# Kernel optimization log

Measured on AMD Instinct MI355X. Metric: run time of the kernel, lower is better.

## Reference

```python
import jax, jax.numpy as jnp
import numpy as np

B, S, E, H, F = 4, 2048, 1024, 16, 4096
D = E // H
EPS = 1e-5


def setup_inputs() -> dict:
    key = jax.random.key(0)
    ks = jax.random.split(key, 12)
    sc_e = 1.0 / np.sqrt(E)
    sc_f = 1.0 / np.sqrt(F)
    inp = {
        'x': jax.random.normal(ks[0], (B, S, E), jnp.float32),
        'mask': jnp.tril(jnp.ones((S, S), jnp.int32))[None, None],  # causal [1,1,S,S]
        'ln1_g': jnp.ones((E,), jnp.float32),
        'ln1_b': jnp.zeros((E,), jnp.float32),
        'Wq': jax.random.normal(ks[1], (E, E), jnp.float32) * sc_e,
        'bq': jnp.zeros((E,), jnp.float32),
        'Wk': jax.random.normal(ks[2], (E, E), jnp.float32) * sc_e,
        'bk': jnp.zeros((E,), jnp.float32),
        'Wv': jax.random.normal(ks[3], (E, E), jnp.float32) * sc_e,
        'bv': jnp.zeros((E,), jnp.float32),
        'Wo': jax.random.normal(ks[4], (E, E), jnp.float32) * sc_e,
        'bo': jnp.zeros((E,), jnp.float32),
        'ln2_g': jnp.ones((E,), jnp.float32),
        'ln2_b': jnp.zeros((E,), jnp.float32),
        'W1': jax.random.normal(ks[5], (F, E), jnp.float32) * sc_e,
        'b1': jnp.zeros((F,), jnp.float32),
        'W2': jax.random.normal(ks[6], (E, F), jnp.float32) * sc_f,
        'b2': jnp.zeros((E,), jnp.float32),
    }
    return inp


def _ln(x, g, b):
    m = jnp.mean(x, axis=-1, keepdims=True)
    v = jnp.mean(jnp.square(x - m), axis=-1, keepdims=True)
    return (x - m) * jax.lax.rsqrt(v + EPS) * g + b


def _attn(h, mask, Wq, bq, Wk, bk, Wv, bv, Wo, bo):
    b, s, _ = h.shape
    q = (h @ Wq.T + bq).reshape(b, s, H, D)
    k = (h @ Wk.T + bk).reshape(b, s, H, D)
    v = (h @ Wv.T + bv).reshape(b, s, H, D)
    scores = jnp.einsum('bqhd,bkhd->bhqk', q, k) / np.sqrt(D)
    scores = jnp.where(mask == 0, -jnp.inf, scores)
    w = jax.nn.softmax(scores, axis=-1)
    ctx = jnp.einsum('bhqk,bkhd->bqhd', w, v).reshape(b, s, E)
    return ctx @ Wo.T + bo


def reference(x, mask, ln1_g, ln1_b, Wq, bq, Wk, bk, Wv, bv, Wo, bo,
              ln2_g, ln2_b, W1, b1, W2, b2):
    x = x + _attn(_ln(x, ln1_g, ln1_b), mask, Wq, bq, Wk, bk, Wv, bv, Wo, bo)
    h = _ln(x, ln2_g, ln2_b)
    ffn = jax.nn.gelu(h @ W1.T + b1, approximate=False) @ W2.T + b2
    return x + ffn
```

## Files before the change

### kernel.cpp

```cpp
#include <hip/hip_runtime.h>
#include <cstdint>
#include <cstddef>

#define E_DIM 1024
#define F_DIM 4096
#define S_LEN 2048
#define NB    4
#define NH    16
#define HD    64
#define MROWS 8192

typedef __bf16 bf16x8 __attribute__((ext_vector_type(8)));
typedef float  f32x4  __attribute__((ext_vector_type(4)));

struct alignas(16) f4 { float x, y, z, w; };
__device__ __forceinline__ f4 ld4(const float* p){ return *(const f4*)p; }

__device__ __forceinline__ unsigned short f2bf(float f){
  union { float f; unsigned int u; } c; c.f = f;
  unsigned int u = c.u;
  return (unsigned short)((u + 0x7FFFu + ((u >> 16) & 1u)) >> 16);
}

__device__ __forceinline__ float gelu_fast(float v){
  const float x  = v * 0.70710678118654752f;
  const float ax = fabsf(x);
  const float t  = __builtin_amdgcn_rcpf(1.0f + 0.3275911f * ax);
  const float p  = t*(0.254829592f + t*(-0.284496736f + t*(1.421413741f +
                   t*(-1.453152027f + t*1.061405429f))));
  float er = 1.0f - p * __expf(-x * x);
  er = (x < 0.0f) ? -er : er;
  return 0.5f * v * (1.0f + er);
}

__device__ __forceinline__ void xcd_swz(int gx, int gy, int& bn, int& bm){
  int fid = blockIdx.y * gx + blockIdx.x;
  const int nwg = gx * gy;
  fid = (fid & 7) * (nwg >> 3) + (fid >> 3);
  bn = fid % gx; bm = fid / gx;
}

__global__ void cvt_kernel(const float* __restrict__ in, unsigned short* __restrict__ out,
                           int n, float scale){
  int i = (blockIdx.x * 256 + threadIdx.x) * 4;
  if (i >= n) return;
  f4 f = ld4(in + i);
  ushort4 o;
  o.x = f2bf(f.x * scale); o.y = f2bf(f.y * scale);
  o.z = f2bf(f.z * scale); o.w = f2bf(f.w * scale);
  *(ushort4*)(out + i) = o;
}

__global__ void bias_cat(const float* __restrict__ bq, const float* __restrict__ bk,
                         const float* __restrict__ bv, float* __restrict__ out, float qsc){
  int i = blockIdx.x * 256 + threadIdx.x;
  if (i >= 3 * E_DIM) return;
  float v = (i < E_DIM) ? bq[i] * qsc : (i < 2 * E_DIM ? bk[i - E_DIM] : bv[i - 2 * E_DIM]);
  out[i] = v;
}

__global__ __launch_bounds__(256) void ln_kernel(const float* __restrict__ in,
                                                 const float* __restrict__ g,
                                                 const float* __restrict__ b,
                                                 unsigned short* __restrict__ out){
  const int row = blockIdx.x;
  const int t = threadIdx.x;
  const float* xr = in + (size_t)row * E_DIM;
  f4 xv = ld4(xr + t * 4);
  float s  = xv.x + xv.y + xv.z + xv.w;
  float ss = xv.x*xv.x + xv.y*xv.y + xv.z*xv.z + xv.w*xv.w;
  #pragma unroll
  for (int o = 1; o < 64; o <<= 1){ s += __shfl_xor(s, o); ss += __shfl_xor(ss, o); }
  __shared__ float sa[4], sb[4];
  if ((t & 63) == 0){ sa[t >> 6] = s; sb[t >> 6] = ss; }
  __syncthreads();
  s  = sa[0] + sa[1] + sa[2] + sa[3];
  ss = sb[0] + sb[1] + sb[2] + sb[3];
  const float mean = s * (1.0f / E_DIM);
  const float var  = ss * (1.0f / E_DIM) - mean * mean;
  const float rstd = rsqrtf(var + 1e-5f);
  f4 gv = ld4(g + t * 4);
  f4 bv = ld4(b + t * 4);
  ushort4 o;
  o.x = f2bf((xv.x - mean) * rstd * gv.x + bv.x);
  o.y = f2bf((xv.y - mean) * rstd * gv.y + bv.y);
  o.z = f2bf((xv.z - mean) * rstd * gv.z + bv.z);
  o.w = f2bf((xv.w - mean) * rstd * gv.w + bv.w);
  *(ushort4*)(out + (size_t)row * E_DIM + t * 4) = o;
}

__device__ __forceinline__ void async_cp16(const unsigned short* g, unsigned short* l){
  __builtin_amdgcn_global_load_lds((const __attribute__((address_space(1))) unsigned int*)g,
                                   (__attribute__((address_space(3)))       unsigned int*)l,
                                   16, 0, 0);
}

template<int EPI>
__global__ __launch_bounds__(256) void gemm_bt(const unsigned short* __restrict__ A,
                                               const unsigned short* __restrict__ W,
                                               const float* __restrict__ bias,
                                               const float* __restrict__ res,
                                               void* __restrict__ outp,
                                               int M, int N, int K){
  __shared__ unsigned short As[128 * 64];
  __shared__ unsigned short Bs[128 * 64];
  int bn, bm; xcd_swz(gridDim.x, gridDim.y, bn, bm);
  const int tid = threadIdx.x;
  const int wv = tid >> 6, lane = tid & 63;
  const int lr = lane & 15, qd = lane >> 4;
  const int wm = (wv >> 1) * 64, wn = (wv & 1) * 64;

  f32x4 acc[4][4];
  #pragma unroll
  for (int mt = 0; mt < 4; ++mt)
    #pragma unroll
    for (int nt = 0; nt < 4; ++nt)
      acc[mt][nt] = f32x4{0.f, 0.f, 0.f, 0.f};

  int soff[4];
  int srow[4];
  #pragma unroll
  for (int it = 0; it < 4; ++it){
    const int cc = tid + it * 256;
    srow[it] = cc >> 3;
    soff[it] = (((cc & 7) ^ (srow[it] & 7))) * 8;
  }
  const unsigned short* Abase = A + (size_t)(bm * 128) * K;
  const unsigned short* Wbase = W + (size_t)(bn * 128) * K;

  for (int k0 = 0; k0 < K; k0 += 64){
    __syncthreads();
    #pragma unroll
    for (int it = 0; it < 4; ++it){
      async_cp16(Abase + (size_t)srow[it] * K + k0 + soff[it], &As[(tid + it * 256) * 8]);
      async_cp16(Wbase + (size_t)srow[it] * K + k0 + soff[it], &Bs[(tid + it * 256) * 8]);
    }
    __builtin_amdgcn_s_waitcnt(0);
    __syncthreads();

    #pragma unroll
    for (int kk = 0; kk < 2; ++kk){
      bf16x8 af[4], bf[4];
      #pragma unroll
      for (int mt = 0; mt < 4; ++mt){
        const int fr = wm + mt * 16 + lr;
        af[mt] = *(const bf16x8*)&As[fr * 64 + (((kk * 4 + qd) ^ (fr & 7))) * 8];
      }
      #pragma unroll
      for (int nt = 0; nt < 4; ++nt){
        const int fr = wn + nt * 16 + lr;
        bf[nt] = *(const bf16x8*)&Bs[fr * 64 + (((kk * 4 + qd) ^ (fr & 7))) * 8];
      }
      #pragma unroll
      for (int mt = 0; mt < 4; ++mt)
        #pragma unroll
        for (int nt = 0; nt < 4; ++nt)
          acc[mt][nt] = __builtin_amdgcn_mfma_f32_16x16x32_bf16(af[mt], bf[nt], acc[mt][nt], 0, 0, 0);
    }
  }

  #pragma unroll
  for (int mt = 0; mt < 4; ++mt){
    #pragma unroll
    for (int r = 0; r < 4; ++r){
      const int gm = bm * 128 + wm + mt * 16 + qd * 4 + r;
      const size_t rowoff = (size_t)gm * N;
      #pragma unroll
      for (int nt = 0; nt < 4; ++nt){
        const int gn = bn * 128 + wn + nt * 16 + lr;
        float v = acc[mt][nt][r] + bias[gn];
        if constexpr (EPI == 1) v = gelu_fast(v);
        if constexpr (EPI == 2) ((float*)outp)[rowoff + gn] = v + res[rowoff + gn];
        else                    ((unsigned short*)outp)[rowoff + gn] = f2bf(v);
      }
    }
  }
}

#define VMW4() asm volatile("s_waitcnt vmcnt(4)" ::: "memory")
#define VMW0() asm volatile("s_waitcnt vmcnt(0)" ::: "memory")
#define BAR()  __builtin_amdgcn_s_barrier()

template<int EPI>
__global__ __launch_bounds__(512, 2) void gemm256(const unsigned short* __restrict__ A,
                                                  const unsigned short* __restrict__ W,
                                                  const float* __restrict__ bias,
                                                  unsigned short* __restrict__ outp,
                                                  int M, int N, int K){
  __shared__ unsigned short lds[2][2][256 * 64];
  const int bn = blockIdx.x, bm = blockIdx.y;
  const int tid = threadIdx.x;
  const int lane = tid & 63;
  const int wv = tid >> 6;
  const int lr = lane & 15, qd = lane >> 4;
  const int wm = wv >> 2, wn = wv & 3;
  const int NT = K >> 6;

  f32x4 acc[2][2][4][2];
  #pragma unroll
  for (int a = 0; a < 2; ++a)
    #pragma unroll
    for (int b = 0; b < 2; ++b)
      #pragma unroll
      for (int c = 0; c < 4; ++c)
        #pragma unroll
        for (int d = 0; d < 2; ++d)
          acc[a][b][c][d] = f32x4{0.f, 0.f, 0.f, 0.f};

  const int srow = tid >> 3;
  const int scol = ((tid & 7) ^ (srow & 7)) * 8;
  const unsigned short* Ab = A + (size_t)(bm * 256 + srow) * K + scol;
  const unsigned short* Wb = W + (size_t)(bn * 256 + srow) * K + scol;

#define STAGE_A(bufi, h, kt) do{ \
    async_cp16(Ab + (size_t)((h)*128     ) * K + (size_t)(kt) * 64, &lds[bufi][0][((h)*128     ) * 64 + tid * 8]); \
    async_cp16(Ab + (size_t)((h)*128 + 64) * K + (size_t)(kt) * 64, &lds[bufi][0][((h)*128 + 64) * 64 + tid * 8]); \
  }while(0)
#define STAGE_B(bufi, h, kt) do{ \
    async_cp16(Wb + (size_t)((h)*128     ) * K + (size_t)(kt) * 64, &lds[bufi][1][((h)*128     ) * 64 + tid * 8]); \
    async_cp16(Wb + (size_t)((h)*128 + 64) * K + (size_t)(kt) * 64, &lds[bufi][1][((h)*128 + 64) * 64 + tid * 8]); \
  }while(0)

  const int sw0 = ((qd    ) ^ (lr & 7)) * 8;
  const int sw1 = ((qd + 4) ^ (lr & 7)) * 8;
  const int arow = wm * 64 + lr;
  const int brow = wn * 32 + lr;

  bf16x8 af[4][2], b0[2][2], b1[2][2];

#define LDA(bufi, mh) do{ \
    _Pragma("unroll") \
    for (int mt = 0; mt < 4; ++mt){ \
      const int r_ = (mh)*128 + arow + mt * 16; \
      af[mt][0] = *(const bf16x8*)&lds[bufi][0][r_ * 64 + sw0]; \
      af[mt][1] = *(const bf16x8*)&lds[bufi][0][r_ * 64 + sw1]; \
    } }while(0)
#define LDB(bufi, nh, dst) do{ \
    _Pragma("unroll") \
    for (int nt = 0; nt < 2; ++nt){ \
      const int r_ = (nh)*128 + brow + nt * 16; \
      dst[nt][0] = *(const bf16x8*)&lds[bufi][1][r_ * 64 + sw0]; \
      dst[nt][1] = *(const bf16x8*)&lds[bufi][1][r_ * 64 + sw1]; \
    } }while(0)
#define MMA(mh, nh, bfr) do{ \
    __builtin_amdgcn_s_setprio(1); \
    _Pragma("unroll") \
    for (int kk = 0; kk < 2; ++kk) \
      _Pragma("unroll") \
      for (int mt = 0; mt < 4; ++mt) \
        _Pragma("unroll") \
        for (int nt = 0; nt < 2; ++nt) \
          acc[mh][nh][mt][nt] = __builtin_amdgcn_mfma_f32_16x16x32_bf16(af[mt][kk], bfr[nt][kk], acc[mh][nh][mt][nt], 0, 0, 0); \
    __builtin_amdgcn_s_setprio(0); \
  }while(0)

  STAGE_A(0, 0, 0); STAGE_B(0, 1, 0); STAGE_A(0, 1, 0); STAGE_B(0, 0, 0);
  STAGE_A(1, 0, 1); STAGE_B(1, 1, 1);
  VMW4(); BAR();

  for (int t = 0; t < NT; t += 2){
    const bool s2 = (t + 2) < NT, s3 = (t + 3) < NT;
    LDA(0, 0); LDB(0, 0, b0);
    STAGE_A(1, 1, t + 1);
    BAR(); MMA(0, 0, b0);
    LDB(0, 1, b1);
    BAR();
    STAGE_B(1, 0, t + 1);
    BAR(); MMA(0, 1, b1);
    LDA(0, 1);
    BAR();
    if (s2) STAGE_A(0, 0, t + 2);
    BAR(); MMA(1, 1, b1); BAR();
    if (s2) STAGE_B(0, 1, t + 2);
    BAR(); MMA(1, 0, b0);
    if (s2) { VMW4(); } else { VMW0(); }
    LDA(1, 0);
    BAR();
    LDB(1, 0, b0);
    if (s2) STAGE_A(0, 1, t + 2);
    BAR(); MMA(0, 0, b0);
    LDB(1, 1, b1);
    BAR();
    if (s2) STAGE_B(0, 0, t + 2);
    BAR(); MMA(0, 1, b1);
    LDA(1, 1);
    BAR();
    if (s3) STAGE_A(1, 0, t + 3);
    BAR(); MMA(1, 1, b1); BAR();
    if (s3) STAGE_B(1, 1, t + 3);
    BAR(); MMA(1, 0, b0);
    VMW4();
    BAR();
  }

  #pragma unroll
  for (int mh = 0; mh < 2; ++mh)
    #pragma unroll
    for (int nh = 0; nh < 2; ++nh)
      #pragma unroll
      for (int mt = 0; mt < 4; ++mt){
        const int gm0 = bm * 256 + mh * 128 + wm * 64 + mt * 16 + qd * 4;
        #pragma unroll
        for (int r = 0; r < 4; ++r){
          const size_t rowoff = (size_t)(gm0 + r) * N;
          #pragma unroll
          for (int nt = 0; nt < 2; ++nt){
            const int gn = bn * 256 + nh * 128 + wn * 32 + nt * 16 + lr;
            float v = acc[mh][nh][mt][nt][r] + bias[gn];
            if constexpr (EPI == 1) v = gelu_fast(v);
            outp[rowoff + gn] = f2bf(v);
          }
        }
      }
#undef STAGE_A
#undef STAGE_B
#undef LDA
#undef LDB
#undef MMA
}

__global__ __launch_bounds__(256) void vtrans(const unsigned short* __restrict__ QKV,
                                              unsigned short* __restrict__ Vt){
  __shared__ unsigned short Ts[64 * 66];
  const int st = blockIdx.x;
  const int h = blockIdx.y, b = blockIdx.z;
  const int tid = threadIdx.x;
  const size_t srcbase = (size_t)(b * S_LEN + st * 64) * 3072 + 2 * E_DIM + h * HD;
  #pragma unroll
  for (int it = 0; it < 4; ++it){
    const int ch = tid + it * 256;
    const int row = ch >> 4, c4 = (ch & 15) * 4;
    *(ushort4*)&Ts[row * 66 + c4] = *(const ushort4*)(QKV + srcbase + (size_t)row * 3072 + c4);
  }
  __syncthreads();
  const size_t dstbase = (size_t)((b * NH + h) * HD) * S_LEN + st * 64;
  #pragma unroll
  for (int it = 0; it < 4; ++it){
    const int ch = tid + it * 256;
    const int d = ch >> 4, t4 = (ch & 15) * 4;
    ushort4 o;
    o.x = Ts[(t4 + 0) * 66 + d];
    o.y = Ts[(t4 + 1) * 66 + d];
    o.z = Ts[(t4 + 2) * 66 + d];
    o.w = Ts[(t4 + 3) * 66 + d];
    *(ushort4*)&Vt[dstbase + (size_t)d * S_LEN + t4] = o;
  }
}

#define AST 72
__global__ __launch_bounds__(256) void attn_mfma(const unsigned short* __restrict__ QKV,
                                                 const unsigned short* __restrict__ Vt,
                                                 unsigned short* __restrict__ Om){
  __shared__ unsigned short Ks[64 * AST];
  __shared__ unsigned short Vs[64 * AST];
  __shared__ unsigned short Ps[64 * AST];
  const int pairi = blockIdx.x;
  const int h = blockIdx.y, b = blockIdx.z;
  const int tid = threadIdx.x;
  const int w = tid >> 6, lane = tid & 63;
  const int lr = lane & 15, qd = lane >> 4;
  const size_t row0 = (size_t)b * S_LEN;
  const int qcol = h * HD;
  const int kcol = E_DIM + h * HD;
  const unsigned short* Vtb = Vt + (size_t)((b * NH + h) * HD) * S_LEN;

  bf16x8 ones;
  #pragma unroll
  for (int j = 0; j < 8; ++j) ones[j] = (__bf16)1.0f;

  for (int ph = 0; ph < 2; ++ph){
    const int qb_t = ph ? (31 - pairi) : pairi;
    const int q0 = qb_t * 64 + w * 16;

    bf16x8 qf[2];
    #pragma unroll
    for (int kk = 0; kk < 2; ++kk)
      qf[kk] = *(const bf16x8*)(QKV + (row0 + q0 + lr) * 3072 + qcol + kk * 32 + qd * 8);

    f32x4 accd[4];
    #pragma unroll
    for (int dt = 0; dt < 4; ++dt) accd[dt] = f32x4{0.f, 0.f, 0.f, 0.f};
    f32x4 lacc = f32x4{0.f, 0.f, 0.f, 0.f};

    for (int kt = 0; kt <= qb_t; ++kt){
      __syncthreads();
      #pragma unroll
      for (int it = 0; it < 2; ++it){
        const int ch = tid + it * 256;
        const int r_ = ch >> 3, c8 = (ch & 7) * 8;
        *(uint4*)&Ks[r_ * AST + c8] = *(const uint4*)(QKV + (row0 + kt * 64 + r_) * 3072 + kcol + c8);
        *(uint4*)&Vs[r_ * AST + c8] = *(const uint4*)(Vtb + (size_t)r_ * S_LEN + kt * 64 + c8);
      }
      __syncthreads();

      f32x4 s[4];
      #pragma unroll
      for (int nt = 0; nt < 4; ++nt) s[nt] = f32x4{0.f, 0.f, 0.f, 0.f};
      #pragma unroll
      for (int kk = 0; kk < 2; ++kk){
        bf16x8 kf[4];
        #pragma unroll
        for (int nt = 0; nt < 4; ++nt)
          kf[nt] = *(const bf16x8*)&Ks[(nt * 16 + lr) * AST + kk * 32 + qd * 8];
        #pragma unroll
        for (int nt = 0; nt < 4; ++nt)
          s[nt] = __builtin_amdgcn_mfma_f32_16x16x32_bf16(qf[kk], kf[nt], s[nt], 0, 0, 0);
      }
      if (kt == qb_t){
        #pragma unroll
        for (int nt = 0; nt < 4; ++nt)
          #pragma unroll
          for (int r = 0; r < 4; ++r){
            const int q  = q0 + qd * 4 + r;
            const int ky = kt * 64 + nt * 16 + lr;
            if (ky > q) s[nt][r] = -3e38f;
          }
      }
      #pragma unroll
      for (int nt = 0; nt < 4; ++nt)
        #pragma unroll
        for (int r = 0; r < 4; ++r){
          union { float f; unsigned u; } cc;
          cc.f = exp2f(s[nt][r]);
          Ps[(w * 16 + qd * 4 + r) * AST + nt * 16 + lr] = (unsigned short)((cc.u + 0x8000u) >> 16);
        }
      __builtin_amdgcn_s_waitcnt(0xc07f);
      #pragma unroll
      for (int kk = 0; kk < 2; ++kk){
        bf16x8 pf = *(const bf16x8*)&Ps[(w * 16 + lr) * AST + kk * 32 + qd * 8];
        bf16x8 vf[4];
        #pragma unroll
        for (int dt = 0; dt < 4; ++dt)
          vf[dt] = *(const bf16x8*)&Vs[(dt * 16 + lr) * AST + kk * 32 + qd * 8];
        #pragma unroll
        for (int dt = 0; dt < 4; ++dt)
          accd[dt] = __builtin_amdgcn_mfma_f32_16x16x32_bf16(pf, vf[dt], accd[dt], 0, 0, 0);
        lacc = __builtin_amdgcn_mfma_f32_16x16x32_bf16(pf, ones, lacc, 0, 0, 0);
      }
    }

    #pragma unroll
    for (int r = 0; r < 4; ++r){
      const float inv = 1.0f / lacc[r];
      const size_t ro = (row0 + q0 + qd * 4 + r) * E_DIM + qcol;
      #pragma unroll
      for (int dt = 0; dt < 4; ++dt)
        Om[ro + dt * 16 + lr] = f2bf(accd[dt][r] * inv);
    }
  }
}

extern "C" void kernel_launch(void* const* d_in, const int* in_sizes, int n_in,
                              void* d_out, int out_size, void* d_ws, size_t ws_size,
                              hipStream_t stream){
  const float* x    = (const float*)d_in[0];
  const float* ln1g = (const float*)d_in[2];
  const float* ln1b = (const float*)d_in[3];
  const float* Wq   = (const float*)d_in[4];
  const float* bq   = (const float*)d_in[5];
  const float* Wk   = (const float*)d_in[6];
  const float* bk   = (const float*)d_in[7];
  const float* Wv   = (const float*)d_in[8];
  const float* bv   = (const float*)d_in[9];
  const float* Wo   = (const float*)d_in[10];
  const float* bo   = (const float*)d_in[11];
  const float* ln2g = (const float*)d_in[12];
  const float* ln2b = (const float*)d_in[13];
  const float* W1   = (const float*)d_in[14];
  const float* b1   = (const float*)d_in[15];
  const float* W2   = (const float*)d_in[16];
  const float* b2   = (const float*)d_in[17];

  char* ws = (char*)d_ws;
  const size_t MB = 1024 * 1024;
  unsigned short* Wqkv_b = (unsigned short*)(ws + 0 * MB);
  unsigned short* Wo_b   = (unsigned short*)(ws + 6 * MB);
  unsigned short* W1_b   = (unsigned short*)(ws + 8 * MB);
  unsigned short* W2_b   = (unsigned short*)(ws + 16 * MB);
  unsigned short* qkvb   = (unsigned short*)(ws + 24 * MB);
  float*          bqkv   = (float*)(ws + 72 * MB);
  unsigned short* Vt_g   = (unsigned short*)(ws + 72 * MB);
  unsigned short* lnb    = (unsigned short*)(ws + 88 * MB);
  float*          xres   = (float*)(ws + 104 * MB);
  unsigned short* ffn1   = (unsigned short*)(ws + 24 * MB);
  unsigned short* ctxb   = lnb;

  const float QSC = 0.125f * 1.4426950408889634f;

  cvt_kernel<<<1024, 256, 0, stream>>>(Wq, Wqkv_b,                   E_DIM * E_DIM, QSC);
  cvt_kernel<<<1024, 256, 0, stream>>>(Wk, Wqkv_b + E_DIM * E_DIM,   E_DIM * E_DIM, 1.0f);
  cvt_kernel<<<1024, 256, 0, stream>>>(Wv, Wqkv_b + 2 * E_DIM * E_DIM, E_DIM * E_DIM, 1.0f);
  cvt_kernel<<<1024, 256, 0, stream>>>(Wo, Wo_b, E_DIM * E_DIM, 1.0f);
  cvt_kernel<<<4096, 256, 0, stream>>>(W1, W1_b, F_DIM * E_DIM, 1.0f);
  cvt_kernel<<<4096, 256, 0, stream>>>(W2, W2_b, F_DIM * E_DIM, 1.0f);
  bias_cat<<<12, 256, 0, stream>>>(bq, bk, bv, bqkv, QSC);

  ln_kernel<<<MROWS, 256, 0, stream>>>(x, ln1g, ln1b, lnb);

  gemm256<0><<<dim3(3 * E_DIM / 256, MROWS / 256), 512, 0, stream>>>(
      lnb, Wqkv_b, bqkv, qkvb, MROWS, 3 * E_DIM, E_DIM);

  vtrans<<<dim3(S_LEN / 64, NH, NB), 256, 0, stream>>>(qkvb, Vt_g);

  attn_mfma<<<dim3(16, NH, NB), 256, 0, stream>>>(qkvb, Vt_g, ctxb);

  gemm_bt<2><<<dim3(E_DIM / 128, MROWS / 128), 256, 0, stream>>>(
      ctxb, Wo_b, bo, x, xres, MROWS, E_DIM, E_DIM);

  ln_kernel<<<MROWS, 256, 0, stream>>>(xres, ln2g, ln2b, lnb);

  gemm256<1><<<dim3(F_DIM / 256, MROWS / 256), 512, 0, stream>>>(
      lnb, W1_b, b1, ffn1, MROWS, F_DIM, E_DIM);

  gemm_bt<2><<<dim3(E_DIM / 128, MROWS / 128), 256, 0, stream>>>(
      ffn1, W2_b, b2, xres, (float*)d_out, MROWS, E_DIM, F_DIM);
}
```

Measured before the change: 517.3 us.

## Prefetch next K/V tile into registers and XOR-swizzle attention LDS

Attention kernel now loads the next K and V tiles into registers while the current tile is being computed, and stores them to shared memory at the start of the next iteration. This hides global load latency behind MFMA work. Shared K/V buffers drop padding in favour of an XOR swizzle on 16-byte chunks to avoid bank conflicts. Register pressure rises slightly.

```diff
diff --git a/kernel.cpp b/kernel.cpp
--- a/kernel.cpp
+++ b/kernel.cpp
@@ -351,8 +351,8 @@
 __global__ __launch_bounds__(256) void attn_mfma(const unsigned short* __restrict__ QKV,
                                                  const unsigned short* __restrict__ Vt,
                                                  unsigned short* __restrict__ Om){
-  __shared__ unsigned short Ks[64 * AST];
-  __shared__ unsigned short Vs[64 * AST];
+  __shared__ unsigned short Ks[64 * 64];
+  __shared__ unsigned short Vs[64 * 64];
   __shared__ unsigned short Ps[64 * AST];
   const int pairi = blockIdx.x;
   const int h = blockIdx.y, b = blockIdx.z;
@@ -364,6 +364,10 @@
   const int kcol = E_DIM + h * HD;
   const unsigned short* Vtb = Vt + (size_t)((b * NH + h) * HD) * S_LEN;
 
+  const int sr  = tid >> 3;
+  const int sc  = (((tid & 7) ^ (sr & 7))) * 8;
+  const int sdst = sr * 64 + (tid & 7) * 8;
+
   bf16x8 ones;
   #pragma unroll
   for (int j = 0; j < 8; ++j) ones[j] = (__bf16)1.0f;
@@ -382,14 +386,23 @@
     for (int dt = 0; dt < 4; ++dt) accd[dt] = f32x4{0.f, 0.f, 0.f, 0.f};
     f32x4 lacc = f32x4{0.f, 0.f, 0.f, 0.f};
 
+    uint4 k0r = *(const uint4*)(QKV + (row0 + sr) * 3072 + kcol + sc);
+    uint4 k1r = *(const uint4*)(QKV + (row0 + sr + 32) * 3072 + kcol + sc);
+    uint4 v0r = *(const uint4*)(Vtb + (size_t)sr * S_LEN + sc);
+    uint4 v1r = *(const uint4*)(Vtb + (size_t)(sr + 32) * S_LEN + sc);
+
     for (int kt = 0; kt <= qb_t; ++kt){
       __syncthreads();
-      #pragma unroll
-      for (int it = 0; it < 2; ++it){
-        const int ch = tid + it * 256;
-        const int r_ = ch >> 3, c8 = (ch & 7) * 8;
-        *(uint4*)&Ks[r_ * AST + c8] = *(const uint4*)(QKV + (row0 + kt * 64 + r_) * 3072 + kcol + c8);
-        *(uint4*)&Vs[r_ * AST + c8] = *(const uint4*)(Vtb + (size_t)r_ * S_LEN + kt * 64 + c8);
+      *(uint4*)&Ks[sdst          ] = k0r;
+      *(uint4*)&Ks[sdst + 32 * 64] = k1r;
+      *(uint4*)&Vs[sdst          ] = v0r;
+      *(uint4*)&Vs[sdst + 32 * 64] = v1r;
+      if (kt < qb_t){
+        const int kn = kt + 1;
+        k0r = *(const uint4*)(QKV + (row0 + kn * 64 + sr) * 3072 + kcol + sc);
+        k1r = *(const uint4*)(QKV + (row0 + kn * 64 + sr + 32) * 3072 + kcol + sc);
+        v0r = *(const uint4*)(Vtb + (size_t)sr * S_LEN + kn * 64 + sc);
+        v1r = *(const uint4*)(Vtb + (size_t)(sr + 32) * S_LEN + kn * 64 + sc);
       }
       __syncthreads();
 
@@ -401,7 +414,7 @@
         bf16x8 kf[4];
         #pragma unroll
         for (int nt = 0; nt < 4; ++nt)
-          kf[nt] = *(const bf16x8*)&Ks[(nt * 16 + lr) * AST + kk * 32 + qd * 8];
+          kf[nt] = *(const bf16x8*)&Ks[(nt * 16 + lr) * 64 + (((kk * 4 + qd) ^ (lr & 7))) * 8];
         #pragma unroll
         for (int nt = 0; nt < 4; ++nt)
           s[nt] = __builtin_amdgcn_mfma_f32_16x16x32_bf16(qf[kk], kf[nt], s[nt], 0, 0, 0);
@@ -431,7 +444,7 @@
         bf16x8 vf[4];
         #pragma unroll
         for (int dt = 0; dt < 4; ++dt)
-          vf[dt] = *(const bf16x8*)&Vs[(dt * 16 + lr) * AST + kk * 32 + qd * 8];
+          vf[dt] = *(const bf16x8*)&Vs[(dt * 16 + lr) * 64 + (((kk * 4 + qd) ^ (lr & 7))) * 8];
         #pragma unroll
         for (int dt = 0; dt < 4; ++dt)
           accd[dt] = __builtin_amdgcn_mfma_f32_16x16x32_bf16(pf, vf[dt], accd[dt], 0, 0, 0);
```

Measured after the change: 524.6 us. No clear change (+1.4%).
